# Kernel optimization log

Measured on AMD Instinct MI355X. Metric: run time of the kernel, lower is better.

Reference implementation:

```python
import jax, jax.numpy as jnp
import numpy as np

NDIM = 128
DEPTH = 6
NPASSES = 4
N_NODES = 50000
N_EDGES = 800000
NODE_IN = 5
LN_EPS = 1e-5


def _mlp_params(key, depth, ndim):
    ks = jax.random.split(key, 6)
    s = 0.05
    return dict(
        W1=jax.random.normal(ks[0], (depth, ndim, ndim), jnp.float32) * s,
        b1=jnp.zeros((depth, ndim), jnp.float32),
        W2=jax.random.normal(ks[1], (depth, ndim, ndim), jnp.float32) * s,
        b2=jnp.zeros((depth, ndim), jnp.float32),
        g=jnp.ones((depth, ndim), jnp.float32),
        bt=jnp.zeros((depth, ndim), jnp.float32),
    )


def setup_inputs() -> dict:
    key = jax.random.key(0)
    k = jax.random.split(key, 8)
    v = jax.random.normal(k[0], (1, N_NODES, NODE_IN), jnp.float32)
    ij = jax.random.randint(k[1], (2, N_EDGES), 0, N_NODES, dtype=jnp.int64)
    ep = _mlp_params(k[2], DEPTH, NDIM)
    npar = _mlp_params(k[3], DEPTH, NDIM)
    return {
        'v': v, 'ij': ij,
        'enc_W': jax.random.normal(k[4], (NODE_IN, NDIM), jnp.float32) * 0.05,
        'enc_b': jnp.zeros((NDIM,), jnp.float32),
        'edge_W1': ep['W1'], 'edge_b1': ep['b1'], 'edge_W2': ep['W2'], 'edge_b2': ep['b2'],
        'edge_g': ep['g'], 'edge_bt': ep['bt'],
        'node_W1': npar['W1'], 'node_b1': npar['b1'], 'node_W2': npar['W2'], 'node_b2': npar['b2'],
        'node_g': npar['g'], 'node_bt': npar['bt'],
        'dec_W': jax.random.normal(k[5], (NDIM, NODE_IN), jnp.float32) * 0.05,
        'dec_b': jnp.zeros((NODE_IN,), jnp.float32),
    }


def _res_block(x, W1, b1, W2, b2, g, bt):
    # x + LayerNorm(relu(relu(x W1 + b1) W2 + b2)); dropout is identity (eval)
    h = jax.nn.relu(x @ W1 + b1)
    h = jax.nn.relu(h @ W2 + b2)
    mu = jnp.mean(h, axis=-1, keepdims=True)
    var = jnp.var(h, axis=-1, keepdims=True)
    h = (h - mu) * jax.lax.rsqrt(var + LN_EPS) * g + bt
    return x + h


def _mlp(x, W1, b1, W2, b2, g, bt):
    for i in range(W1.shape[0]):
        x = _res_block(x, W1[i], b1[i], W2[i], b2[i], g[i], bt[i])
    return x


def reference(v, ij, enc_W, enc_b,
              edge_W1, edge_b1, edge_W2, edge_b2, edge_g, edge_bt,
              node_W1, node_b1, node_W2, node_b2, node_g, node_bt,
              dec_W, dec_b):
    ij0, ij1 = ij[0], ij[1]
    h = v @ enc_W + enc_b                      # [B, N, D]
    e = None
    for _ in range(NPASSES):
        # Edge update: gather endpoint features
        x = h[:, ij0] - h[:, ij1]              # [B, E, D]
        if e is not None:
            x = x + e
        e = _mlp(x, edge_W1, edge_b1, edge_W2, edge_b2, edge_g, edge_bt)
        # Node update: scatter-sum edges to destination nodes
        agg = jnp.zeros_like(h).at[:, ij1].add(e)
        h = _mlp(h + agg, node_W1, node_b1, node_W2, node_b2, node_g, node_bt)
    return h @ dec_W + dec_b                   # [B, N, node_input_dim]
```

## Files before the change

### kernel.cpp

```cpp
#include <hip/hip_runtime.h>
#include <hip/hip_bf16.h>
#include <cstdint>
#include <cstddef>

#define NDIMC   128
#define DEPTHC  6
#define NPASSESC 4
#define NNODES  50000
#define NEDGES  800000
#define NODEIN  5
#define LNEPS   1e-5f

#define H_OFF    0ull
#define E_OFF    25600000ull
#define PW_OFF   230400000ull
#define FLAG_OFF 231186432ull
#define DEG_OFF  231186436ull
#define RS_OFF   231386440ull
#define CUR_OFF  231586444ull
#define EIDX_OFF 231786444ull
#define PWMAT    98304

typedef __attribute__((ext_vector_type(8))) short mgn_sh8;
typedef __attribute__((ext_vector_type(4))) float mgn_f32x4;

__device__ __forceinline__ unsigned mgn_bf16bits(float f) {
    unsigned x = __float_as_uint(f);
    return (x + 0x7fffu + ((x >> 16) & 1u)) >> 16;
}
__device__ __forceinline__ unsigned mgn_pk(float a, float b) {
    __hip_bfloat162 t = __float22bfloat162_rn(make_float2(a, b));
    union { __hip_bfloat162 h; unsigned u; } c; c.h = t; return c.u;
}

__device__ __forceinline__ void mgn_cp16(const unsigned short* g, unsigned short* l) {
    __builtin_amdgcn_global_load_lds(
        (const __attribute__((address_space(1))) void*)g,
        (__attribute__((address_space(3))) void*)l, 16, 0, 0);
}
template <int BW>
__device__ __forceinline__ void mgn_stage_half(const unsigned short* __restrict__ src,
                                               unsigned short* wbuf, int tid) {
    const int w = tid >> 6, l = tid & 63;
#pragma unroll
    for (int i = 0; i < 16 / BW; ++i) {
        const int off = (w * (16 / BW) + i) * 512 + l * 8;
        mgn_cp16(src + off, wbuf + off);
    }
}

__global__ void mgn_detect_kernel(const int* __restrict__ ij, int* __restrict__ flag) {
    __shared__ int any;
    if (threadIdx.x == 0) any = 0;
    __syncthreads();
    if (ij[2 * threadIdx.x + 1] != 0) atomicOr(&any, 1);
    __syncthreads();
    if (threadIdx.x == 0) *flag = any;
}

__device__ __forceinline__ long mgn_load_idx(const int* __restrict__ ij, long pos, int is32) {
    if (is32) return (long)ij[pos];
    const long long* ij8 = (const long long*)ij;
    return (long)ij8[pos];
}

__global__ void mgn_pack_kernel(const float* __restrict__ W, unsigned short* __restrict__ pw) {
    int i = blockIdx.x * blockDim.x + threadIdx.x;
    if (i >= PWMAT) return;
    int j    = i & 7;
    int lane = (i >> 3) & 63;
    int sp   = (i >> 9) & 1;
    int t    = (i >> 10) & 7;
    int sh   = (i >> 13) & 1;
    int d    = i >> 14;
    int k = (sh * 2 + sp) * 32 + (lane >> 4) * 8 + j;
    int n = (lane & 15) * 8 + t;
    pw[i] = (unsigned short)mgn_bf16bits(W[(d * NDIMC + k) * NDIMC + n]);
}

__global__ void mgn_deg_kernel(const int* __restrict__ ij, const int* __restrict__ flag,
                               int* __restrict__ deg) {
    int e = blockIdx.x * blockDim.x + threadIdx.x;
    if (e >= NEDGES) return;
    int dst = (int)mgn_load_idx(ij, (long)NEDGES + e, *flag);
    atomicAdd(&deg[dst], 1);
}

__global__ void mgn_scan_kernel(const int* __restrict__ deg,
                                int* __restrict__ rowstart, int* __restrict__ cursor) {
    __shared__ int partial[256];
    const int tid = threadIdx.x;
    const int CH = (NNODES + 255) / 256;
    const int base = tid * CH;
    int s = 0;
    for (int i = 0; i < CH; ++i) {
        int idx = base + i;
        if (idx < NNODES) s += deg[idx];
    }
    partial[tid] = s;
    __syncthreads();
    for (int off = 1; off < 256; off <<= 1) {
        int add = (tid >= off) ? partial[tid - off] : 0;
        __syncthreads();
        partial[tid] += add;
        __syncthreads();
    }
    int run = (tid == 0) ? 0 : partial[tid - 1];
    for (int i = 0; i < CH; ++i) {
        int idx = base + i;
        if (idx < NNODES) {
            rowstart[idx] = run;
            cursor[idx]   = run;
            run += deg[idx];
        }
    }
    if (tid == 255) rowstart[NNODES] = run;
}

__global__ void mgn_fill_kernel(const int* __restrict__ ij, const int* __restrict__ flag,
                                int* __restrict__ cursor, int* __restrict__ eidx) {
    int e = blockIdx.x * blockDim.x + threadIdx.x;
    if (e >= NEDGES) return;
    int dst = (int)mgn_load_idx(ij, (long)NEDGES + e, *flag);
    int pos = atomicAdd(&cursor[dst], 1);
    eidx[pos] = e;
}

__global__ void mgn_encoder_kernel(const float* __restrict__ v,
                                   const float* __restrict__ encW,
                                   const float* __restrict__ encB,
                                   float* __restrict__ h) {
    int idx = blockIdx.x * blockDim.x + threadIdx.x;
    if (idx >= NNODES * NDIMC) return;
    int n = idx >> 7, d = idx & 127;
    float acc = encB[d];
#pragma unroll
    for (int k = 0; k < NODEIN; ++k)
        acc = fmaf(v[n * NODEIN + k], encW[k * NDIMC + d], acc);
    h[idx] = acc;
}

__global__ void mgn_decoder_kernel(const float* __restrict__ h,
                                   const float* __restrict__ decW,
                                   const float* __restrict__ decB,
                                   float* __restrict__ out) {
    int idx = blockIdx.x * blockDim.x + threadIdx.x;
    if (idx >= NNODES * NODEIN) return;
    int n = idx / NODEIN, j = idx % NODEIN;
    float acc = decB[j];
#pragma unroll 8
    for (int k = 0; k < NDIMC; ++k)
        acc = fmaf(h[n * NDIMC + k], decW[k * NODEIN + j], acc);
    out[idx] = acc;
}

template <int MODE, int BW>
__global__ __launch_bounds__(BW * 64, 2) void mgn_mlp6_mfma_kernel(
    float* __restrict__ Xf,
    unsigned short* __restrict__ Eb,
    const float* __restrict__ H,
    const int* __restrict__ ij,
    const int* __restrict__ flag,
    const int* __restrict__ rowstart,
    const int* __restrict__ eidx,
    int addE, int nrows,
    const unsigned short* __restrict__ PW1,
    const unsigned short* __restrict__ PW2,
    const float* __restrict__ B1, const float* __restrict__ B2,
    const float* __restrict__ G,  const float* __restrict__ BT)
{
    __shared__ unsigned short xl[BW * 16 * 136];
    __shared__ unsigned short wb0[8192];
    __shared__ unsigned short wb1[8192];
    const int tid = threadIdx.x;
    const int w   = tid >> 6;
    const int l   = tid & 63;
    const int q   = l >> 4;
    const int lm  = l & 15;
    const int ct  = lm * 8;
    const int wbase = w * 16;
    const long rowbase = (long)blockIdx.x * (16 * BW);

    const int is32 = (MODE == 1) ? *flag : 0;

    mgn_stage_half<BW>(PW1, wb0, tid);

    float xres[4][8];
#pragma unroll
    for (int r = 0; r < 4; ++r) {
        const int rloc = wbase + q * 4 + r;
        long gr = rowbase + rloc;
        bool ok = gr < nrows;
        float xv[8];
#pragma unroll
        for (int t = 0; t < 8; ++t) xv[t] = 0.f;
        if (MODE == 1) {
            if (ok) {
                long er = (long)eidx[gr];
                long i0 = mgn_load_idx(ij, er, is32);
                long i1 = mgn_load_idx(ij, (long)NEDGES + er, is32);
                const float* p0 = H + i0 * NDIMC + ct;
                const float* p1 = H + i1 * NDIMC + ct;
                float4 a0 = *(const float4*)p0, a1 = *(const float4*)(p0 + 4);
                float4 b0 = *(const float4*)p1, b1 = *(const float4*)(p1 + 4);
                xv[0] = a0.x - b0.x; xv[1] = a0.y - b0.y;
                xv[2] = a0.z - b0.z; xv[3] = a0.w - b0.w;
                xv[4] = a1.x - b1.x; xv[5] = a1.y - b1.y;
                xv[6] = a1.z - b1.z; xv[7] = a1.w - b1.w;
                if (addE) {
                    uint4 u4 = *(const uint4*)(Eb + (size_t)gr * NDIMC + ct);
                    xv[0] += __uint_as_float(u4.x << 16);
                    xv[1] += __uint_as_float(u4.x & 0xffff0000u);
                    xv[2] += __uint_as_float(u4.y << 16);
                    xv[3] += __uint_as_float(u4.y & 0xffff0000u);
                    xv[4] += __uint_as_float(u4.z << 16);
                    xv[5] += __uint_as_float(u4.z & 0xffff0000u);
                    xv[6] += __uint_as_float(u4.w << 16);
                    xv[7] += __uint_as_float(u4.w & 0xffff0000u);
                }
            }
        } else {
            if (ok) {
                float4 a0 = *(const float4*)(Xf + gr * NDIMC + ct);
                float4 a1 = *(const float4*)(Xf + gr * NDIMC + ct + 4);
                xv[0] = a0.x; xv[1] = a0.y; xv[2] = a0.z; xv[3] = a0.w;
                xv[4] = a1.x; xv[5] = a1.y; xv[6] = a1.z; xv[7] = a1.w;
                int rs = rowstart[gr], re = rowstart[gr + 1];
                for (int k = rs; k < re; ++k) {
                    uint4 u4 = *(const uint4*)(Eb + (size_t)k * NDIMC + ct);
                    xv[0] += __uint_as_float(u4.x << 16);
                    xv[1] += __uint_as_float(u4.x & 0xffff0000u);
                    xv[2] += __uint_as_float(u4.y << 16);
                    xv[3] += __uint_as_float(u4.y & 0xffff0000u);
                    xv[4] += __uint_as_float(u4.z << 16);
                    xv[5] += __uint_as_float(u4.z & 0xffff0000u);
                    xv[6] += __uint_as_float(u4.w << 16);
                    xv[7] += __uint_as_float(u4.w & 0xffff0000u);
                }
            }
        }
#pragma unroll
        for (int t = 0; t < 8; ++t) xres[r][t] = xv[t];
        uint4 pk;
        pk.x = mgn_pk(xv[0], xv[1]); pk.y = mgn_pk(xv[2], xv[3]);
        pk.z = mgn_pk(xv[4], xv[5]); pk.w = mgn_pk(xv[6], xv[7]);
        *(uint4*)&xl[rloc * 136 + ct] = pk;
    }

    __syncthreads();

    mgn_sh8 a[4];
    mgn_f32x4 acc[8];
    const int arow = (wbase + lm) * 136;

    for (int d = 0; d < DEPTHC; ++d) {
        const unsigned short* pw1 = PW1 + (size_t)(d * 2) * 8192;
        const unsigned short* pw2 = PW2 + (size_t)(d * 2) * 8192;

        mgn_stage_half<BW>(pw1 + 8192, wb1, tid);

        float4 b1a = *(const float4*)(B1 + d * NDIMC + ct);
        float4 b1b = *(const float4*)(B1 + d * NDIMC + ct + 4);
        float b1v[8] = {b1a.x, b1a.y, b1a.z, b1a.w, b1b.x, b1b.y, b1b.z, b1b.w};

#pragma unroll
        for (int s = 0; s < 4; ++s)
            a[s] = *(const mgn_sh8*)&xl[arow + s * 32 + q * 8];
#pragma unroll
        for (int t = 0; t < 8; ++t)
            acc[t] = (mgn_f32x4){b1v[t], b1v[t], b1v[t], b1v[t]};
#pragma unroll
        for (int t = 0; t < 8; ++t)
#pragma unroll
            for (int sp = 0; sp < 2; ++sp) {
                mgn_sh8 b = *(const mgn_sh8*)&wb0[(t * 2 + sp) * 512 + l * 8];
                acc[t] = __builtin_amdgcn_mfma_f32_16x16x32_bf16(a[sp], b, acc[t], 0, 0, 0);
            }
        __syncthreads();

        mgn_stage_half<BW>(pw2, wb0, tid);
#pragma unroll
        for (int t = 0; t < 8; ++t)
#pragma unroll
            for (int sp = 0; sp < 2; ++sp) {
                mgn_sh8 b = *(const mgn_sh8*)&wb1[(t * 2 + sp) * 512 + l * 8];
                acc[t] = __builtin_amdgcn_mfma_f32_16x16x32_bf16(a[2 + sp], b, acc[t], 0, 0, 0);
            }
#pragma unroll
        for (int r = 0; r < 4; ++r) {
            const int rloc = wbase + q * 4 + r;
            float h1[8];
#pragma unroll
            for (int t = 0; t < 8; ++t) h1[t] = fmaxf(acc[t][r], 0.f);
            uint4 pk;
            pk.x = mgn_pk(h1[0], h1[1]); pk.y = mgn_pk(h1[2], h1[3]);
            pk.z = mgn_pk(h1[4], h1[5]); pk.w = mgn_pk(h1[6], h1[7]);
            *(uint4*)&xl[rloc * 136 + ct] = pk;
        }
        __syncthreads();

        mgn_stage_half<BW>(pw2 + 8192, wb1, tid);

        float4 b2a = *(const float4*)(B2 + d * NDIMC + ct);
        float4 b2b = *(const float4*)(B2 + d * NDIMC + ct + 4);
        float4 ga  = *(const float4*)(G  + d * NDIMC + ct);
        float4 gb  = *(const float4*)(G  + d * NDIMC + ct + 4);
        float4 bta = *(const float4*)(BT + d * NDIMC + ct);
        float4 btb = *(const float4*)(BT + d * NDIMC + ct + 4);
        float b2v[8] = {b2a.x, b2a.y, b2a.z, b2a.w, b2b.x, b2b.y, b2b.z, b2b.w};
        float gv[8]  = {ga.x, ga.y, ga.z, ga.w, gb.x, gb.y, gb.z, gb.w};
        float btv[8] = {bta.x, bta.y, bta.z, bta.w, btb.x, btb.y, btb.z, btb.w};

#pragma unroll
        for (int s = 0; s < 4; ++s)
            a[s] = *(const mgn_sh8*)&xl[arow + s * 32 + q * 8];
#pragma unroll
        for (int t = 0; t < 8; ++t)
            acc[t] = (mgn_f32x4){b2v[t], b2v[t], b2v[t], b2v[t]};
#pragma unroll
        for (int t = 0; t < 8; ++t)
#pragma unroll
            for (int sp = 0; sp < 2; ++sp) {
                mgn_sh8 b = *(const mgn_sh8*)&wb0[(t * 2 + sp) * 512 + l * 8];
                acc[t] = __builtin_amdgcn_mfma_f32_16x16x32_bf16(a[sp], b, acc[t], 0, 0, 0);
            }
        __syncthreads();

        if (d + 1 < DEPTHC)
            mgn_stage_half<BW>(PW1 + (size_t)((d + 1) * 2) * 8192, wb0, tid);
#pragma unroll
        for (int t = 0; t < 8; ++t)
#pragma unroll
            for (int sp = 0; sp < 2; ++sp) {
                mgn_sh8 b = *(const mgn_sh8*)&wb1[(t * 2 + sp) * 512 + l * 8];
                acc[t] = __builtin_amdgcn_mfma_f32_16x16x32_bf16(a[2 + sp], b, acc[t], 0, 0, 0);
            }
#pragma unroll
        for (int r = 0; r < 4; ++r) {
            const int rloc = wbase + q * 4 + r;
            float h2[8];
#pragma unroll
            for (int t = 0; t < 8; ++t) h2[t] = fmaxf(acc[t][r], 0.f);
            float sum = 0.f, ssq = 0.f;
#pragma unroll
            for (int t = 0; t < 8; ++t) {
                sum += h2[t];
                ssq = fmaf(h2[t], h2[t], ssq);
            }
            sum += __shfl_xor(sum, 1); ssq += __shfl_xor(ssq, 1);
            sum += __shfl_xor(sum, 2); ssq += __shfl_xor(ssq, 2);
            sum += __shfl_xor(sum, 4); ssq += __shfl_xor(ssq, 4);
            sum += __shfl_xor(sum, 8); ssq += __shfl_xor(ssq, 8);
            float mean = sum * 0.0078125f;
            float var  = fmaf(-mean, mean, ssq * 0.0078125f);
            float rstd = rsqrtf(var + LNEPS);
#pragma unroll
            for (int t = 0; t < 8; ++t) {
                float at = rstd * gv[t];
                float ctt = fmaf(-mean, at, btv[t]);
                xres[r][t] += fmaf(h2[t], at, ctt);
            }
            if (d != DEPTHC - 1) {
                uint4 pk;
                pk.x = mgn_pk(xres[r][0], xres[r][1]);
                pk.y = mgn_pk(xres[r][2], xres[r][3]);
                pk.z = mgn_pk(xres[r][4], xres[r][5]);
                pk.w = mgn_pk(xres[r][6], xres[r][7]);
                *(uint4*)&xl[rloc * 136 + ct] = pk;
            }
        }
        if (d + 1 < DEPTHC) __syncthreads();
    }

#pragma unroll
    for (int r = 0; r < 4; ++r) {
        const int rloc = wbase + q * 4 + r;
        long gr = rowbase + rloc;
        if (gr < nrows) {
            if (MODE == 1) {
                uint4 pk;
                pk.x = mgn_pk(xres[r][0], xres[r][1]);
                pk.y = mgn_pk(xres[r][2], xres[r][3]);
                pk.z = mgn_pk(xres[r][4], xres[r][5]);
                pk.w = mgn_pk(xres[r][6], xres[r][7]);
                *(uint4*)(Eb + (size_t)gr * NDIMC + ct) = pk;
            } else {
                float4 a0 = {xres[r][0], xres[r][1], xres[r][2], xres[r][3]};
                float4 a1 = {xres[r][4], xres[r][5], xres[r][6], xres[r][7]};
                *(float4*)(Xf + gr * NDIMC + ct)     = a0;
                *(float4*)(Xf + gr * NDIMC + ct + 4) = a1;
            }
        }
    }
}

extern "C" void kernel_launch(void* const* d_in, const int* in_sizes, int n_in,
                              void* d_out, int out_size, void* d_ws, size_t ws_size,
                              hipStream_t stream) {
    const float* v    = (const float*)d_in[0];
    const int*   ij   = (const int*)d_in[1];
    const float* encW = (const float*)d_in[2];
    const float* encB = (const float*)d_in[3];
    const float* eW1  = (const float*)d_in[4];
    const float* eB1  = (const float*)d_in[5];
    const float* eW2  = (const float*)d_in[6];
    const float* eB2  = (const float*)d_in[7];
    const float* eG   = (const float*)d_in[8];
    const float* eBT  = (const float*)d_in[9];
    const float* nW1  = (const float*)d_in[10];
    const float* nB1  = (const float*)d_in[11];
    const float* nW2  = (const float*)d_in[12];
    const float* nB2  = (const float*)d_in[13];
    const float* nG   = (const float*)d_in[14];
    const float* nBT  = (const float*)d_in[15];
    const float* decW = (const float*)d_in[16];
    const float* decB = (const float*)d_in[17];
    float* out = (float*)d_out;

    char* ws = (char*)d_ws;
    float*          h    = (float*)(ws + H_OFF);
    unsigned short* ebuf = (unsigned short*)(ws + E_OFF);
    unsigned short* pw   = (unsigned short*)(ws + PW_OFF);
    int*            flag = (int*)(ws + FLAG_OFF);
    int*            deg  = (int*)(ws + DEG_OFF);
    int*            rstt = (int*)(ws + RS_OFF);
    int*            curs = (int*)(ws + CUR_OFF);
    int*            eidx = (int*)(ws + EIDX_OFF);

    mgn_detect_kernel<<<1, 256, 0, stream>>>(ij, flag);
    mgn_pack_kernel<<<(PWMAT + 255) / 256, 256, 0, stream>>>(eW1, pw + 0 * PWMAT);
    mgn_pack_kernel<<<(PWMAT + 255) / 256, 256, 0, stream>>>(eW2, pw + 1 * PWMAT);
    mgn_pack_kernel<<<(PWMAT + 255) / 256, 256, 0, stream>>>(nW1, pw + 2 * PWMAT);
    mgn_pack_kernel<<<(PWMAT + 255) / 256, 256, 0, stream>>>(nW2, pw + 3 * PWMAT);

    hipMemsetAsync(deg, 0, (size_t)(NNODES + 1) * sizeof(int), stream);
    mgn_deg_kernel<<<(NEDGES + 255) / 256, 256, 0, stream>>>(ij, flag, deg);
    mgn_scan_kernel<<<1, 256, 0, stream>>>(deg, rstt, curs);
    mgn_fill_kernel<<<(NEDGES + 255) / 256, 256, 0, stream>>>(ij, flag, curs, eidx);

    mgn_encoder_kernel<<<(NNODES * NDIMC + 255) / 256, 256, 0, stream>>>(v, encW, encB, h);

    for (int p = 0; p < NPASSESC; ++p) {
        mgn_mlp6_mfma_kernel<1, 4><<<NEDGES / 64, 256, 0, stream>>>(
            nullptr, ebuf, h, ij, flag, nullptr, eidx, p > 0 ? 1 : 0, NEDGES,
            pw + 0 * PWMAT, pw + 1 * PWMAT, eB1, eB2, eG, eBT);
        mgn_mlp6_mfma_kernel<0, 4><<<(NNODES + 63) / 64, 256, 0, stream>>>(
            h, ebuf, nullptr, nullptr, nullptr, rstt, nullptr, 0, NNODES,
            pw + 2 * PWMAT, pw + 3 * PWMAT, nB1, nB2, nG, nBT);
    }

    mgn_decoder_kernel<<<(NNODES * NODEIN + 255) / 256, 256, 0, stream>>>(h, decW, decB, out);
}
```

Before: 3.313 ms.

## Load MLP weight fragments directly from global into registers, drop LDS staging

Removes the LDS double-buffered staging of packed bf16 weights and the block-wide barriers around it. Each wave now reads its MFMA B fragments straight from global (L1/L2-cached) with a one-step register prefetch across output tiles. Since each wave only touches its own rows of xl, the __syncthreads are dropped, and the launch bound is raised to 3 blocks per SM to use the freed LDS. The trade-off is that every wave re-reads all weights from cache instead of sharing one LDS copy, which adds L1/L2 traffic and register pressure.

New measurement: 3.903 ms. 17.8% more time.

```diff
diff --git a/kernel.cpp b/kernel.cpp
--- a/kernel.cpp
+++ b/kernel.cpp
@@ -31,22 +31,6 @@
 __device__ __forceinline__ unsigned mgn_pk(float a, float b) {
     __hip_bfloat162 t = __float22bfloat162_rn(make_float2(a, b));
     union { __hip_bfloat162 h; unsigned u; } c; c.h = t; return c.u;
-}
-
-__device__ __forceinline__ void mgn_cp16(const unsigned short* g, unsigned short* l) {
-    __builtin_amdgcn_global_load_lds(
-        (const __attribute__((address_space(1))) void*)g,
-        (__attribute__((address_space(3))) void*)l, 16, 0, 0);
-}
-template <int BW>
-__device__ __forceinline__ void mgn_stage_half(const unsigned short* __restrict__ src,
-                                               unsigned short* wbuf, int tid) {
-    const int w = tid >> 6, l = tid & 63;
-#pragma unroll
-    for (int i = 0; i < 16 / BW; ++i) {
-        const int off = (w * (16 / BW) + i) * 512 + l * 8;
-        mgn_cp16(src + off, wbuf + off);
-    }
 }
 
 __global__ void mgn_detect_kernel(const int* __restrict__ ij, int* __restrict__ flag) {
@@ -155,7 +139,7 @@
 }
 
 template <int MODE, int BW>
-__global__ __launch_bounds__(BW * 64, 2) void mgn_mlp6_mfma_kernel(
+__global__ __launch_bounds__(BW * 64, 3) void mgn_mlp6_mfma_kernel(
     float* __restrict__ Xf,
     unsigned short* __restrict__ Eb,
     const float* __restrict__ H,
@@ -170,8 +154,6 @@
     const float* __restrict__ G,  const float* __restrict__ BT)
 {
     __shared__ unsigned short xl[BW * 16 * 136];
-    __shared__ unsigned short wb0[8192];
-    __shared__ unsigned short wb1[8192];
     const int tid = threadIdx.x;
     const int w   = tid >> 6;
     const int l   = tid & 63;
@@ -182,8 +164,6 @@
     const long rowbase = (long)blockIdx.x * (16 * BW);
 
     const int is32 = (MODE == 1) ? *flag : 0;
-
-    mgn_stage_half<BW>(PW1, wb0, tid);
 
     float xres[4][8];
 #pragma unroll
@@ -247,17 +227,13 @@
         *(uint4*)&xl[rloc * 136 + ct] = pk;
     }
 
-    __syncthreads();
-
     mgn_sh8 a[4];
     mgn_f32x4 acc[8];
     const int arow = (wbase + lm) * 136;
 
     for (int d = 0; d < DEPTHC; ++d) {
-        const unsigned short* pw1 = PW1 + (size_t)(d * 2) * 8192;
-        const unsigned short* pw2 = PW2 + (size_t)(d * 2) * 8192;
-
-        mgn_stage_half<BW>(pw1 + 8192, wb1, tid);
+        const unsigned short* pw1 = PW1 + (size_t)d * 16384;
+        const unsigned short* pw2 = PW2 + (size_t)d * 16384;
 
         float4 b1a = *(const float4*)(B1 + d * NDIMC + ct);
         float4 b1b = *(const float4*)(B1 + d * NDIMC + ct + 4);
@@ -269,23 +245,26 @@
 #pragma unroll
         for (int t = 0; t < 8; ++t)
             acc[t] = (mgn_f32x4){b1v[t], b1v[t], b1v[t], b1v[t]};
-#pragma unroll
-        for (int t = 0; t < 8; ++t)
-#pragma unroll
-            for (int sp = 0; sp < 2; ++sp) {
-                mgn_sh8 b = *(const mgn_sh8*)&wb0[(t * 2 + sp) * 512 + l * 8];
-                acc[t] = __builtin_amdgcn_mfma_f32_16x16x32_bf16(a[sp], b, acc[t], 0, 0, 0);
-            }
-        __syncthreads();
-
-        mgn_stage_half<BW>(pw2, wb0, tid);
-#pragma unroll
-        for (int t = 0; t < 8; ++t)
-#pragma unroll
-            for (int sp = 0; sp < 2; ++sp) {
-                mgn_sh8 b = *(const mgn_sh8*)&wb1[(t * 2 + sp) * 512 + l * 8];
-                acc[t] = __builtin_amdgcn_mfma_f32_16x16x32_bf16(a[2 + sp], b, acc[t], 0, 0, 0);
-            }
+        {
+            mgn_sh8 bc[4], bn[4];
+#pragma unroll
+            for (int kb = 0; kb < 4; ++kb)
+                bc[kb] = *(const mgn_sh8*)&pw1[(kb >> 1) * 8192 + (kb & 1) * 512 + l * 8];
+#pragma unroll
+            for (int t = 0; t < 8; ++t) {
+                if (t < 7) {
+#pragma unroll
+                    for (int kb = 0; kb < 4; ++kb)
+                        bn[kb] = *(const mgn_sh8*)&pw1[(kb >> 1) * 8192 + ((t + 1) * 2 + (kb & 1)) * 512 + l * 8];
+                }
+#pragma unroll
+                for (int kb = 0; kb < 4; ++kb)
+                    acc[t] = __builtin_amdgcn_mfma_f32_16x16x32_bf16(a[kb], bc[kb], acc[t], 0, 0, 0);
+#pragma unroll
+                for (int kb = 0; kb < 4; ++kb) bc[kb] = bn[kb];
+            }
+        }
+
 #pragma unroll
         for (int r = 0; r < 4; ++r) {
             const int rloc = wbase + q * 4 + r;
@@ -297,9 +276,6 @@
             pk.z = mgn_pk(h1[4], h1[5]); pk.w = mgn_pk(h1[6], h1[7]);
             *(uint4*)&xl[rloc * 136 + ct] = pk;
         }
-        __syncthreads();
-
-        mgn_stage_half<BW>(pw2 + 8192, wb1, tid);
 
         float4 b2a = *(const float4*)(B2 + d * NDIMC + ct);
         float4 b2b = *(const float4*)(B2 + d * NDIMC + ct + 4);
@@ -317,24 +293,26 @@
 #pragma unroll
         for (int t = 0; t < 8; ++t)
             acc[t] = (mgn_f32x4){b2v[t], b2v[t], b2v[t], b2v[t]};
-#pragma unroll
-        for (int t = 0; t < 8; ++t)
-#pragma unroll
-            for (int sp = 0; sp < 2; ++sp) {
-                mgn_sh8 b = *(const mgn_sh8*)&wb0[(t * 2 + sp) * 512 + l * 8];
-                acc[t] = __builtin_amdgcn_mfma_f32_16x16x32_bf16(a[sp], b, acc[t], 0, 0, 0);
-            }
-        __syncthreads();
-
-        if (d + 1 < DEPTHC)
-            mgn_stage_half<BW>(PW1 + (size_t)((d + 1) * 2) * 8192, wb0, tid);
-#pragma unroll
-        for (int t = 0; t < 8; ++t)
-#pragma unroll
-            for (int sp = 0; sp < 2; ++sp) {
-                mgn_sh8 b = *(const mgn_sh8*)&wb1[(t * 2 + sp) * 512 + l * 8];
-                acc[t] = __builtin_amdgcn_mfma_f32_16x16x32_bf16(a[2 + sp], b, acc[t], 0, 0, 0);
-            }
+        {
+            mgn_sh8 bc[4], bn[4];
+#pragma unroll
+            for (int kb = 0; kb < 4; ++kb)
+                bc[kb] = *(const mgn_sh8*)&pw2[(kb >> 1) * 8192 + (kb & 1) * 512 + l * 8];
+#pragma unroll
+            for (int t = 0; t < 8; ++t) {
+                if (t < 7) {
+#pragma unroll
+                    for (int kb = 0; kb < 4; ++kb)
+                        bn[kb] = *(const mgn_sh8*)&pw2[(kb >> 1) * 8192 + ((t + 1) * 2 + (kb & 1)) * 512 + l * 8];
+                }
+#pragma unroll
+                for (int kb = 0; kb < 4; ++kb)
+                    acc[t] = __builtin_amdgcn_mfma_f32_16x16x32_bf16(a[kb], bc[kb], acc[t], 0, 0, 0);
+#pragma unroll
+                for (int kb = 0; kb < 4; ++kb) bc[kb] = bn[kb];
+            }
+        }
+
 #pragma unroll
         for (int r = 0; r < 4; ++r) {
             const int rloc = wbase + q * 4 + r;
@@ -369,7 +347,6 @@
                 *(uint4*)&xl[rloc * 136 + ct] = pk;
             }
         }
-        if (d + 1 < DEPTHC) __syncthreads();
     }
 
 #pragma unroll
```

## Stage MLP weights in quarter tiles to raise occupancy, add XCD swizzle and DPP reductions

Applied to the files above, without the earlier changes.

Weight staging now uses two 8 KB quarter buffers in place of two 16 KB half buffers. That cuts LDS per block, and launch bounds go from 2 to 4 blocks per CU to hide gather and staging latency, at the cost of more barriers per layer. Block indices are remapped so each XCD handles a contiguous range of rows. The LayerNorm reductions use DPP adds in place of most shuffles, and the MFMA sections raise wave priority.

After: 2.826 ms (median of 2 runs). 14.7% less time.

```diff
diff --git a/kernel.cpp b/kernel.cpp
--- a/kernel.cpp
+++ b/kernel.cpp
@@ -33,20 +33,47 @@
     union { __hip_bfloat162 h; unsigned u; } c; c.h = t; return c.u;
 }
 
+template <int CTRL>
+__device__ __forceinline__ float mgn_dppadd(float x) {
+    int y = __builtin_amdgcn_update_dpp(0, __float_as_int(x), CTRL, 0xF, 0xF, true);
+    return x + __int_as_float(y);
+}
+
+__device__ __forceinline__ int mgn_swz(int orig, int nwg) {
+    int qq = nwg >> 3, rr = nwg & 7;
+    int xcd = orig & 7, idx = orig >> 3;
+    int base = (xcd < rr) ? xcd * (qq + 1) : rr * (qq + 1) + (xcd - rr) * qq;
+    return base + idx;
+}
+
 __device__ __forceinline__ void mgn_cp16(const unsigned short* g, unsigned short* l) {
     __builtin_amdgcn_global_load_lds(
         (const __attribute__((address_space(1))) void*)g,
         (__attribute__((address_space(3))) void*)l, 16, 0, 0);
 }
 template <int BW>
-__device__ __forceinline__ void mgn_stage_half(const unsigned short* __restrict__ src,
-                                               unsigned short* wbuf, int tid) {
+__device__ __forceinline__ void mgn_stage_q(const unsigned short* __restrict__ src,
+                                            unsigned short* wbuf, int tid) {
     const int w = tid >> 6, l = tid & 63;
 #pragma unroll
-    for (int i = 0; i < 16 / BW; ++i) {
-        const int off = (w * (16 / BW) + i) * 512 + l * 8;
+    for (int i = 0; i < 8 / BW; ++i) {
+        const int off = (w * (8 / BW) + i) * 512 + l * 8;
         mgn_cp16(src + off, wbuf + off);
     }
+}
+
+template <int TQ>
+__device__ __forceinline__ void mgn_qcompT(const unsigned short* __restrict__ buf, int l,
+                                           const mgn_sh8* ap, mgn_f32x4* acc) {
+    __builtin_amdgcn_s_setprio(1);
+#pragma unroll
+    for (int t = 0; t < 4; ++t)
+#pragma unroll
+        for (int sp = 0; sp < 2; ++sp) {
+            mgn_sh8 b = *(const mgn_sh8*)&buf[(t * 2 + sp) * 512 + l * 8];
+            acc[TQ + t] = __builtin_amdgcn_mfma_f32_16x16x32_bf16(ap[sp], b, acc[TQ + t], 0, 0, 0);
+        }
+    __builtin_amdgcn_s_setprio(0);
 }
 
 __global__ void mgn_detect_kernel(const int* __restrict__ ij, int* __restrict__ flag) {
@@ -155,7 +182,7 @@
 }
 
 template <int MODE, int BW>
-__global__ __launch_bounds__(BW * 64, 2) void mgn_mlp6_mfma_kernel(
+__global__ __launch_bounds__(BW * 64, 4) void mgn_mlp6_mfma_kernel(
     float* __restrict__ Xf,
     unsigned short* __restrict__ Eb,
     const float* __restrict__ H,
@@ -170,8 +197,8 @@
     const float* __restrict__ G,  const float* __restrict__ BT)
 {
     __shared__ unsigned short xl[BW * 16 * 136];
-    __shared__ unsigned short wb0[8192];
-    __shared__ unsigned short wb1[8192];
+    __shared__ unsigned short wqA[4096];
+    __shared__ unsigned short wqB[4096];
     const int tid = threadIdx.x;
     const int w   = tid >> 6;
     const int l   = tid & 63;
@@ -179,11 +206,12 @@
     const int lm  = l & 15;
     const int ct  = lm * 8;
     const int wbase = w * 16;
-    const long rowbase = (long)blockIdx.x * (16 * BW);
+    const int bid = mgn_swz((int)blockIdx.x, (int)gridDim.x);
+    const long rowbase = (long)bid * (16 * BW);
 
     const int is32 = (MODE == 1) ? *flag : 0;
 
-    mgn_stage_half<BW>(PW1, wb0, tid);
+    mgn_stage_q<BW>(PW1, wqA, tid);
 
     float xres[4][8];
 #pragma unroll
@@ -254,38 +282,32 @@
     const int arow = (wbase + lm) * 136;
 
     for (int d = 0; d < DEPTHC; ++d) {
-        const unsigned short* pw1 = PW1 + (size_t)(d * 2) * 8192;
-        const unsigned short* pw2 = PW2 + (size_t)(d * 2) * 8192;
-
-        mgn_stage_half<BW>(pw1 + 8192, wb1, tid);
-
-        float4 b1a = *(const float4*)(B1 + d * NDIMC + ct);
-        float4 b1b = *(const float4*)(B1 + d * NDIMC + ct + 4);
-        float b1v[8] = {b1a.x, b1a.y, b1a.z, b1a.w, b1b.x, b1b.y, b1b.z, b1b.w};
+        const unsigned short* pw1 = PW1 + (size_t)d * 16384;
+        const unsigned short* pw2 = PW2 + (size_t)d * 16384;
 
 #pragma unroll
         for (int s = 0; s < 4; ++s)
             a[s] = *(const mgn_sh8*)&xl[arow + s * 32 + q * 8];
-#pragma unroll
-        for (int t = 0; t < 8; ++t)
-            acc[t] = (mgn_f32x4){b1v[t], b1v[t], b1v[t], b1v[t]};
-#pragma unroll
-        for (int t = 0; t < 8; ++t)
-#pragma unroll
-            for (int sp = 0; sp < 2; ++sp) {
-                mgn_sh8 b = *(const mgn_sh8*)&wb0[(t * 2 + sp) * 512 + l * 8];
-                acc[t] = __builtin_amdgcn_mfma_f32_16x16x32_bf16(a[sp], b, acc[t], 0, 0, 0);
-            }
-        __syncthreads();
-
-        mgn_stage_half<BW>(pw2, wb0, tid);
-#pragma unroll
-        for (int t = 0; t < 8; ++t)
-#pragma unroll
-            for (int sp = 0; sp < 2; ++sp) {
-                mgn_sh8 b = *(const mgn_sh8*)&wb1[(t * 2 + sp) * 512 + l * 8];
-                acc[t] = __builtin_amdgcn_mfma_f32_16x16x32_bf16(a[2 + sp], b, acc[t], 0, 0, 0);
-            }
+        {
+            float4 ba = *(const float4*)(B1 + d * NDIMC + ct);
+            float4 bb = *(const float4*)(B1 + d * NDIMC + ct + 4);
+            float bv[8] = {ba.x, ba.y, ba.z, ba.w, bb.x, bb.y, bb.z, bb.w};
+#pragma unroll
+            for (int t = 0; t < 8; ++t)
+                acc[t] = (mgn_f32x4){bv[t], bv[t], bv[t], bv[t]};
+        }
+
+        mgn_stage_q<BW>(pw1 + 4096, wqB, tid);
+        mgn_qcompT<0>(wqA, l, a + 0, acc);
+        __syncthreads();
+        mgn_stage_q<BW>(pw1 + 8192, wqA, tid);
+        mgn_qcompT<4>(wqB, l, a + 0, acc);
+        __syncthreads();
+        mgn_stage_q<BW>(pw1 + 12288, wqB, tid);
+        mgn_qcompT<0>(wqA, l, a + 2, acc);
+        __syncthreads();
+        mgn_stage_q<BW>(pw2, wqA, tid);
+        mgn_qcompT<4>(wqB, l, a + 2, acc);
 #pragma unroll
         for (int r = 0; r < 4; ++r) {
             const int rloc = wbase + q * 4 + r;
@@ -297,76 +319,71 @@
             pk.z = mgn_pk(h1[4], h1[5]); pk.w = mgn_pk(h1[6], h1[7]);
             *(uint4*)&xl[rloc * 136 + ct] = pk;
         }
-        __syncthreads();
-
-        mgn_stage_half<BW>(pw2 + 8192, wb1, tid);
-
-        float4 b2a = *(const float4*)(B2 + d * NDIMC + ct);
-        float4 b2b = *(const float4*)(B2 + d * NDIMC + ct + 4);
-        float4 ga  = *(const float4*)(G  + d * NDIMC + ct);
-        float4 gb  = *(const float4*)(G  + d * NDIMC + ct + 4);
-        float4 bta = *(const float4*)(BT + d * NDIMC + ct);
-        float4 btb = *(const float4*)(BT + d * NDIMC + ct + 4);
-        float b2v[8] = {b2a.x, b2a.y, b2a.z, b2a.w, b2b.x, b2b.y, b2b.z, b2b.w};
-        float gv[8]  = {ga.x, ga.y, ga.z, ga.w, gb.x, gb.y, gb.z, gb.w};
-        float btv[8] = {bta.x, bta.y, bta.z, bta.w, btb.x, btb.y, btb.z, btb.w};
-
 #pragma unroll
         for (int s = 0; s < 4; ++s)
             a[s] = *(const mgn_sh8*)&xl[arow + s * 32 + q * 8];
-#pragma unroll
-        for (int t = 0; t < 8; ++t)
-            acc[t] = (mgn_f32x4){b2v[t], b2v[t], b2v[t], b2v[t]};
-#pragma unroll
-        for (int t = 0; t < 8; ++t)
-#pragma unroll
-            for (int sp = 0; sp < 2; ++sp) {
-                mgn_sh8 b = *(const mgn_sh8*)&wb0[(t * 2 + sp) * 512 + l * 8];
-                acc[t] = __builtin_amdgcn_mfma_f32_16x16x32_bf16(a[sp], b, acc[t], 0, 0, 0);
-            }
-        __syncthreads();
-
+        {
+            float4 ba = *(const float4*)(B2 + d * NDIMC + ct);
+            float4 bb = *(const float4*)(B2 + d * NDIMC + ct + 4);
+            float bv[8] = {ba.x, ba.y, ba.z, ba.w, bb.x, bb.y, bb.z, bb.w};
+#pragma unroll
+            for (int t = 0; t < 8; ++t)
+                acc[t] = (mgn_f32x4){bv[t], bv[t], bv[t], bv[t]};
+        }
+        __syncthreads();
+        mgn_stage_q<BW>(pw2 + 4096, wqB, tid);
+        mgn_qcompT<0>(wqA, l, a + 0, acc);
+        __syncthreads();
+        mgn_stage_q<BW>(pw2 + 8192, wqA, tid);
+        mgn_qcompT<4>(wqB, l, a + 0, acc);
+        __syncthreads();
+        mgn_stage_q<BW>(pw2 + 12288, wqB, tid);
+        mgn_qcompT<0>(wqA, l, a + 2, acc);
+        __syncthreads();
         if (d + 1 < DEPTHC)
-            mgn_stage_half<BW>(PW1 + (size_t)((d + 1) * 2) * 8192, wb0, tid);
-#pragma unroll
-        for (int t = 0; t < 8; ++t)
-#pragma unroll
-            for (int sp = 0; sp < 2; ++sp) {
-                mgn_sh8 b = *(const mgn_sh8*)&wb1[(t * 2 + sp) * 512 + l * 8];
-                acc[t] = __builtin_amdgcn_mfma_f32_16x16x32_bf16(a[2 + sp], b, acc[t], 0, 0, 0);
-            }
-#pragma unroll
-        for (int r = 0; r < 4; ++r) {
-            const int rloc = wbase + q * 4 + r;
-            float h2[8];
-#pragma unroll
-            for (int t = 0; t < 8; ++t) h2[t] = fmaxf(acc[t][r], 0.f);
-            float sum = 0.f, ssq = 0.f;
-#pragma unroll
-            for (int t = 0; t < 8; ++t) {
-                sum += h2[t];
-                ssq = fmaf(h2[t], h2[t], ssq);
-            }
-            sum += __shfl_xor(sum, 1); ssq += __shfl_xor(ssq, 1);
-            sum += __shfl_xor(sum, 2); ssq += __shfl_xor(ssq, 2);
-            sum += __shfl_xor(sum, 4); ssq += __shfl_xor(ssq, 4);
-            sum += __shfl_xor(sum, 8); ssq += __shfl_xor(ssq, 8);
-            float mean = sum * 0.0078125f;
-            float var  = fmaf(-mean, mean, ssq * 0.0078125f);
-            float rstd = rsqrtf(var + LNEPS);
-#pragma unroll
-            for (int t = 0; t < 8; ++t) {
-                float at = rstd * gv[t];
-                float ctt = fmaf(-mean, at, btv[t]);
-                xres[r][t] += fmaf(h2[t], at, ctt);
-            }
-            if (d != DEPTHC - 1) {
-                uint4 pk;
-                pk.x = mgn_pk(xres[r][0], xres[r][1]);
-                pk.y = mgn_pk(xres[r][2], xres[r][3]);
-                pk.z = mgn_pk(xres[r][4], xres[r][5]);
-                pk.w = mgn_pk(xres[r][6], xres[r][7]);
-                *(uint4*)&xl[rloc * 136 + ct] = pk;
+            mgn_stage_q<BW>(PW1 + (size_t)(d + 1) * 16384, wqA, tid);
+        mgn_qcompT<4>(wqB, l, a + 2, acc);
+
+        {
+            float4 ga  = *(const float4*)(G  + d * NDIMC + ct);
+            float4 gb  = *(const float4*)(G  + d * NDIMC + ct + 4);
+            float4 bta = *(const float4*)(BT + d * NDIMC + ct);
+            float4 btb = *(const float4*)(BT + d * NDIMC + ct + 4);
+            float gv[8]  = {ga.x, ga.y, ga.z, ga.w, gb.x, gb.y, gb.z, gb.w};
+            float btv[8] = {bta.x, bta.y, bta.z, bta.w, btb.x, btb.y, btb.z, btb.w};
+#pragma unroll
+            for (int r = 0; r < 4; ++r) {
+                const int rloc = wbase + q * 4 + r;
+                float h2[8];
+#pragma unroll
+                for (int t = 0; t < 8; ++t) h2[t] = fmaxf(acc[t][r], 0.f);
+                float sum = 0.f, ssq = 0.f;
+#pragma unroll
+                for (int t = 0; t < 8; ++t) {
+                    sum += h2[t];
+                    ssq = fmaf(h2[t], h2[t], ssq);
+                }
+                sum = mgn_dppadd<0xB1>(sum);  ssq = mgn_dppadd<0xB1>(ssq);
+                sum = mgn_dppadd<0x4E>(sum);  ssq = mgn_dppadd<0x4E>(ssq);
+                sum += __shfl_xor(sum, 4);    ssq += __shfl_xor(ssq, 4);
+                sum = mgn_dppadd<0x128>(sum); ssq = mgn_dppadd<0x128>(ssq);
+                float mean = sum * 0.0078125f;
+                float var  = fmaf(-mean, mean, ssq * 0.0078125f);
+                float rstd = rsqrtf(var + LNEPS);
+#pragma unroll
+                for (int t = 0; t < 8; ++t) {
+                    float at = rstd * gv[t];
+                    float ctt = fmaf(-mean, at, btv[t]);
+                    xres[r][t] += fmaf(h2[t], at, ctt);
+                }
+                if (d != DEPTHC - 1) {
+                    uint4 pk;
+                    pk.x = mgn_pk(xres[r][0], xres[r][1]);
+                    pk.y = mgn_pk(xres[r][2], xres[r][3]);
+                    pk.z = mgn_pk(xres[r][4], xres[r][5]);
+                    pk.w = mgn_pk(xres[r][6], xres[r][7]);
+                    *(uint4*)&xl[rloc * 136 + ct] = pk;
+                }
             }
         }
         if (d + 1 < DEPTHC) __syncthreads();
@@ -385,10 +402,10 @@
                 pk.w = mgn_pk(xres[r][6], xres[r][7]);
                 *(uint4*)(Eb + (size_t)gr * NDIMC + ct) = pk;
             } else {
-                float4 a0 = {xres[r][0], xres[r][1], xres[r][2], xres[r][3]};
-                float4 a1 = {xres[r][4], xres[r][5], xres[r][6], xres[r][7]};
-                *(float4*)(Xf + gr * NDIMC + ct)     = a0;
-                *(float4*)(Xf + gr * NDIMC + ct + 4) = a1;
+                float4 o0 = {xres[r][0], xres[r][1], xres[r][2], xres[r][3]};
+                float4 o1 = {xres[r][4], xres[r][5], xres[r][6], xres[r][7]};
+                *(float4*)(Xf + gr * NDIMC + ct)     = o0;
+                *(float4*)(Xf + gr * NDIMC + ct + 4) = o1;
             }
         }
     }
```
